# Kernel tuning notes

Measured on AMD Instinct MI355X. Metric: run time of the kernel, lower is better.

## Reference

```python
import jax, jax.numpy as jnp
import numpy as np

D = 256          # embedding_dim
N_SUPPORT = 320  # n_way * n_shot = 20 * 16
N_QUERY = 2048
N_WAY = 20


def setup_inputs() -> dict:
    key = jax.random.key(0)
    ks = jax.random.split(key, 6)
    scale = 1.0 / np.sqrt(2 * D)
    return {
        "support_embeddings": jax.random.normal(ks[0], (N_SUPPORT, D), dtype=jnp.float32),
        "query_embeddings": jax.random.normal(ks[1], (N_QUERY, D), dtype=jnp.float32),
        "support_labels": jax.random.randint(ks[2], (N_SUPPORT,), 0, N_WAY, dtype=jnp.int64)
            if jax.config.jax_enable_x64 else jax.random.randint(ks[2], (N_SUPPORT,), 0, N_WAY, dtype=jnp.int32),
        "W1": jax.random.normal(ks[3], (2 * D, D), dtype=jnp.float32) * scale,
        "b1": jax.random.normal(ks[4], (D,), dtype=jnp.float32) * scale,
        "W2": jax.random.normal(ks[5], (D,), dtype=jnp.float32) * (1.0 / np.sqrt(D)),
        "b2": jnp.zeros((1,), dtype=jnp.float32),
        "n_way": N_WAY,
        "n_shot": 16,
    }


def reference(support_embeddings, query_embeddings, support_labels, W1, b1, W2, b2, n_way, n_shot):
    d = support_embeddings.shape[-1]
    # Linear1 over concat([query, support]) == query @ W1[:d] + support @ W1[d:]
    q_proj = query_embeddings @ W1[:d]          # [Q, D]
    s_proj = support_embeddings @ W1[d:]        # [S, D]
    hidden = jax.nn.relu(q_proj[:, None, :] + s_proj[None, :, :] + b1)  # [Q, S, D]
    scores = jnp.einsum("qsd,d->qs", hidden, W2) + b2[0]                # [Q, S]
    weights = jax.nn.softmax(scores, axis=1)                            # softmax over support set
    onehot = jax.nn.one_hot(support_labels, n_way, dtype=weights.dtype) # [S, n_way]
    logits = weights @ onehot                                           # [Q, n_way]
    return logits
```

## Files before the change

### kernel.cpp

```cpp
#include <hip/hip_runtime.h>
#include <cstdint>

#define DD   256
#define NS   320
#define NQ   2048
#define NWAY 20
#define QT   4
#define SBLK 4
#define NQB  (NQ / QT)
#define NSB  (NS / SBLK)
#define MT   640

__global__ __launch_bounds__(256) void proj_kernel(
    const float* __restrict__ sup, const float* __restrict__ qe,
    const float* __restrict__ W1, const float* __restrict__ b1,
    float* __restrict__ qp, float* __restrict__ spbT) {
  const int d = threadIdx.x;
  const int b = blockIdx.x;
  if (b < NQB) {
    const int q0 = b * QT;
    float acc[QT] = {0.f, 0.f, 0.f, 0.f};
    const float* w = W1 + d;
#pragma unroll 8
    for (int k = 0; k < DD; ++k) {
      const float wv = w[(size_t)k * DD];
#pragma unroll
      for (int i = 0; i < QT; ++i)
        acc[i] += qe[(q0 + i) * DD + k] * wv;
    }
#pragma unroll
    for (int i = 0; i < QT; ++i)
      qp[(size_t)(q0 + i) * DD + d] = acc[i];
  } else {
    const int s0 = (b - NQB) * SBLK;
    float acc[SBLK] = {0.f, 0.f, 0.f, 0.f};
    const float* w = W1 + (size_t)DD * DD + d;
#pragma unroll 8
    for (int k = 0; k < DD; ++k) {
      const float wv = w[(size_t)k * DD];
#pragma unroll
      for (int i = 0; i < SBLK; ++i)
        acc[i] += sup[(s0 + i) * DD + k] * wv;
    }
    const float bb = b1[d];
#pragma unroll
    for (int i = 0; i < SBLK; ++i)
      spbT[d * NS + s0 + i] = acc[i] + bb;
  }
}

__global__ __launch_bounds__(MT) void matchnet_kernel(
    const float* __restrict__ qp, const float* __restrict__ spbT,
    const float* __restrict__ W2, const int* __restrict__ labels,
    float* __restrict__ out) {
  __shared__ float qlds[QT * DD];
  __shared__ float wlds[DD];
  __shared__ float part[QT][NS];
  __shared__ float lds_cs[QT * NWAY];
  __shared__ float lds_wm[5];
  const int t  = threadIdx.x;
  const int q0 = blockIdx.x * QT;

  if (t < QT * DD / 4) {
    ((float4*)qlds)[t] = ((const float4*)(qp + (size_t)q0 * DD))[t];
  } else if (t < QT * DD / 4 + DD / 4) {
    const int j = t - QT * DD / 4;
    ((float4*)wlds)[j] = ((const float4*)W2)[j];
  }
  if (t < QT * NWAY) lds_cs[t] = 0.f;
  __syncthreads();

  const int half = t / NS;
  const int s    = t - half * NS;
  const int d0   = half * (DD / 2);
  const int lab  = labels[s];

  float acc[QT] = {0.f, 0.f, 0.f, 0.f};
  const float* pS = spbT + d0 * NS + s;
#pragma unroll 2
  for (int dd = 0; dd < DD / 2; dd += 4) {
    const int d = d0 + dd;
    const float sv0 = pS[(dd + 0) * NS];
    const float sv1 = pS[(dd + 1) * NS];
    const float sv2 = pS[(dd + 2) * NS];
    const float sv3 = pS[(dd + 3) * NS];
    const float4 wv = *(const float4*)(wlds + d);
#pragma unroll
    for (int i = 0; i < QT; ++i) {
      const float4 qv = *(const float4*)(qlds + i * DD + d);
      acc[i] += fmaxf(qv.x + sv0, 0.f) * wv.x
              + fmaxf(qv.y + sv1, 0.f) * wv.y
              + fmaxf(qv.z + sv2, 0.f) * wv.z
              + fmaxf(qv.w + sv3, 0.f) * wv.w;
    }
  }

  if (half) {
#pragma unroll
    for (int i = 0; i < QT; ++i) part[i][s] = acc[i];
  }
  __syncthreads();
  if (!half) {
#pragma unroll
    for (int i = 0; i < QT; ++i) acc[i] += part[i][s];
    float m = acc[0];
#pragma unroll
    for (int i = 1; i < QT; ++i) m = fmaxf(m, acc[i]);
#pragma unroll
    for (int off = 32; off > 0; off >>= 1)
      m = fmaxf(m, __shfl_xor(m, off));
    if ((t & 63) == 0) lds_wm[t >> 6] = m;
  }
  __syncthreads();
  if (!half) {
    float M = lds_wm[0];
#pragma unroll
    for (int w = 1; w < 5; ++w) M = fmaxf(M, lds_wm[w]);
#pragma unroll
    for (int i = 0; i < QT; ++i) {
      const float w = __expf(acc[i] - M);
      atomicAdd(&lds_cs[i * NWAY + lab], w);
    }
  }
  __syncthreads();
  if (t < QT * NWAY) {
    const int i = t / NWAY, c = t - i * NWAY;
    float tot = 0.f;
#pragma unroll
    for (int j = 0; j < NWAY; ++j) tot += lds_cs[i * NWAY + j];
    out[(size_t)(q0 + i) * NWAY + c] = lds_cs[i * NWAY + c] / tot;
  }
}

extern "C" void kernel_launch(void* const* d_in, const int* in_sizes, int n_in,
                              void* d_out, int out_size, void* d_ws, size_t ws_size,
                              hipStream_t stream) {
  const float* sup = (const float*)d_in[0];
  const float* qe  = (const float*)d_in[1];
  const int*   lab = (const int*)d_in[2];
  const float* W1  = (const float*)d_in[3];
  const float* b1  = (const float*)d_in[4];
  const float* W2  = (const float*)d_in[5];
  float* out  = (float*)d_out;
  float* spbT = (float*)d_ws;
  float* qpr  = spbT + (size_t)DD * NS;

  proj_kernel<<<NQB + NSB, 256, 0, stream>>>(sup, qe, W1, b1, qpr, spbT);
  matchnet_kernel<<<NQ / QT, MT, 0, stream>>>(qpr, spbT, W2, lab, out);
}
```

Baseline: 103.2 us.

## Double query tile, split-K projection, scalar-load operands, bucket softmax by label

The query tile in both kernels grows from 4 to 8. That halves the number of matchnet blocks and doubles how often each support-projection load is reused. The projection kernel now splits the K dimension across two 256-thread halves and combines them through LDS. The matchnet kernel reads query and W2 values straight from global memory through wave-uniform (scalar) addresses instead of staging them in LDS. The per-class sum replaces the LDS atomic scatter with a label-bucket index list that is built once per block and then summed. The costs are more registers per thread, a hard CMAX=64 limit on support items per class, and a serial bucket-sum loop.

Result: no change. 101.7 us (-1.5%).

```diff
diff --git a/kernel.cpp b/kernel.cpp
--- a/kernel.cpp
+++ b/kernel.cpp
@@ -5,89 +5,91 @@
 #define NS   320
 #define NQ   2048
 #define NWAY 20
-#define QT   4
-#define SBLK 4
+#define QT   8
 #define NQB  (NQ / QT)
-#define NSB  (NS / SBLK)
-#define MT   640
+#define NSB  (NS / QT)
+#define CMAX 64
 
-__global__ __launch_bounds__(256) void proj_kernel(
+__global__ __launch_bounds__(512) void proj_kernel(
     const float* __restrict__ sup, const float* __restrict__ qe,
     const float* __restrict__ W1, const float* __restrict__ b1,
     float* __restrict__ qp, float* __restrict__ spbT) {
-  const int d = threadIdx.x;
-  const int b = blockIdx.x;
-  if (b < NQB) {
-    const int q0 = b * QT;
-    float acc[QT] = {0.f, 0.f, 0.f, 0.f};
-    const float* w = W1 + d;
+  __shared__ float pacc[QT][DD];
+  const int t  = threadIdx.x;
+  const int d  = t & 255;
+  const int kh = t >> 8;
+  const int b  = blockIdx.x;
+  const bool isQ = (b < NQB);
+  const int r0 = isQ ? b * QT : (b - NQB) * QT;
+  const float* src   = isQ ? qe : sup;
+  const float* wcol  = W1 + (isQ ? 0 : (size_t)DD * DD) + (size_t)(kh * 128) * DD + d;
+  const float* rbase = src + __builtin_amdgcn_readfirstlane(r0 * DD + kh * 128);
+
+  float acc[QT] = {0.f, 0.f, 0.f, 0.f, 0.f, 0.f, 0.f, 0.f};
 #pragma unroll 8
-    for (int k = 0; k < DD; ++k) {
-      const float wv = w[(size_t)k * DD];
+  for (int k = 0; k < 128; ++k) {
+    const float wv = wcol[(size_t)k * DD];
+#pragma unroll
+    for (int i = 0; i < QT; ++i)
+      acc[i] += rbase[i * DD + k] * wv;
+  }
+  if (kh) {
+#pragma unroll
+    for (int i = 0; i < QT; ++i) pacc[i][d] = acc[i];
+  }
+  __syncthreads();
+  if (!kh) {
+    if (isQ) {
 #pragma unroll
       for (int i = 0; i < QT; ++i)
-        acc[i] += qe[(q0 + i) * DD + k] * wv;
+        qp[(size_t)(r0 + i) * DD + d] = acc[i] + pacc[i][d];
+    } else {
+      const float bb = b1[d];
+#pragma unroll
+      for (int i = 0; i < QT; ++i)
+        spbT[d * NS + r0 + i] = acc[i] + pacc[i][d] + bb;
     }
-#pragma unroll
-    for (int i = 0; i < QT; ++i)
-      qp[(size_t)(q0 + i) * DD + d] = acc[i];
-  } else {
-    const int s0 = (b - NQB) * SBLK;
-    float acc[SBLK] = {0.f, 0.f, 0.f, 0.f};
-    const float* w = W1 + (size_t)DD * DD + d;
-#pragma unroll 8
-    for (int k = 0; k < DD; ++k) {
-      const float wv = w[(size_t)k * DD];
-#pragma unroll
-      for (int i = 0; i < SBLK; ++i)
-        acc[i] += sup[(s0 + i) * DD + k] * wv;
-    }
-    const float bb = b1[d];
-#pragma unroll
-    for (int i = 0; i < SBLK; ++i)
-      spbT[d * NS + s0 + i] = acc[i] + bb;
   }
 }
 
-__global__ __launch_bounds__(MT) void matchnet_kernel(
+__global__ __launch_bounds__(640) void matchnet_kernel(
     const float* __restrict__ qp, const float* __restrict__ spbT,
     const float* __restrict__ W2, const int* __restrict__ labels,
     float* __restrict__ out) {
-  __shared__ float qlds[QT * DD];
-  __shared__ float wlds[DD];
-  __shared__ float part[QT][NS];
-  __shared__ float lds_cs[QT * NWAY];
-  __shared__ float lds_wm[5];
-  const int t  = threadIdx.x;
-  const int q0 = blockIdx.x * QT;
-
-  if (t < QT * DD / 4) {
-    ((float4*)qlds)[t] = ((const float4*)(qp + (size_t)q0 * DD))[t];
-  } else if (t < QT * DD / 4 + DD / 4) {
-    const int j = t - QT * DD / 4;
-    ((float4*)wlds)[j] = ((const float4*)W2)[j];
-  }
-  if (t < QT * NWAY) lds_cs[t] = 0.f;
-  __syncthreads();
-
+  __shared__ float wexp[QT][NS];
+  __shared__ float wm[5];
+  __shared__ float csum[QT * NWAY];
+  __shared__ int   ccnt[NWAY];
+  __shared__ short cidx[NWAY * CMAX];
+  const int t    = threadIdx.x;
+  const int q0   = blockIdx.x * QT;
   const int half = t / NS;
   const int s    = t - half * NS;
-  const int d0   = half * (DD / 2);
-  const int lab  = labels[s];
 
-  float acc[QT] = {0.f, 0.f, 0.f, 0.f};
-  const float* pS = spbT + d0 * NS + s;
+  if (t < NWAY) ccnt[t] = 0;
+  __syncthreads();
+  if (!half) {
+    const int lab  = labels[s];
+    const int slot = atomicAdd(&ccnt[lab], 1);
+    cidx[lab * CMAX + slot] = (short)s;
+  }
+
+  const int d0 = half * (DD / 2);
+  const float* qb = qp + __builtin_amdgcn_readfirstlane(q0 * DD + d0);
+  const float* wb = W2 + d0;
+  const float* sb = spbT + (size_t)d0 * NS + s;
+
+  float acc[QT] = {0.f, 0.f, 0.f, 0.f, 0.f, 0.f, 0.f, 0.f};
 #pragma unroll 2
   for (int dd = 0; dd < DD / 2; dd += 4) {
-    const int d = d0 + dd;
-    const float sv0 = pS[(dd + 0) * NS];
-    const float sv1 = pS[(dd + 1) * NS];
-    const float sv2 = pS[(dd + 2) * NS];
-    const float sv3 = pS[(dd + 3) * NS];
-    const float4 wv = *(const float4*)(wlds + d);
+    const float sv0 = sb[(dd + 0) * NS];
+    const float sv1 = sb[(dd + 1) * NS];
+    const float sv2 = sb[(dd + 2) * NS];
+    const float sv3 = sb[(dd + 3) * NS];
+    const float4 wv = *(const float4*)(wb + dd);
 #pragma unroll
     for (int i = 0; i < QT; ++i) {
-      const float4 qv = *(const float4*)(qlds + i * DD + d);
+      const float4 qv = *(const float4*)(qb + i * DD + dd);
       acc[i] += fmaxf(qv.x + sv0, 0.f) * wv.x
               + fmaxf(qv.y + sv1, 0.f) * wv.y
               + fmaxf(qv.z + sv2, 0.f) * wv.z
@@ -97,38 +99,39 @@
 
   if (half) {
 #pragma unroll
-    for (int i = 0; i < QT; ++i) part[i][s] = acc[i];
+    for (int i = 0; i < QT; ++i) wexp[i][s] = acc[i];
+  }
+  __syncthreads();
+  float m = -1e30f;
+  if (!half) {
+#pragma unroll
+    for (int i = 0; i < QT; ++i) { acc[i] += wexp[i][s]; m = fmaxf(m, acc[i]); }
+#pragma unroll
+    for (int off = 32; off > 0; off >>= 1)
+      m = fmaxf(m, __shfl_xor(m, off));
+    if ((t & 63) == 0) wm[t >> 6] = m;
   }
   __syncthreads();
   if (!half) {
+    const float M = fmaxf(fmaxf(fmaxf(wm[0], wm[1]), fmaxf(wm[2], wm[3])), wm[4]);
 #pragma unroll
-    for (int i = 0; i < QT; ++i) acc[i] += part[i][s];
-    float m = acc[0];
-#pragma unroll
-    for (int i = 1; i < QT; ++i) m = fmaxf(m, acc[i]);
-#pragma unroll
-    for (int off = 32; off > 0; off >>= 1)
-      m = fmaxf(m, __shfl_xor(m, off));
-    if ((t & 63) == 0) lds_wm[t >> 6] = m;
+    for (int i = 0; i < QT; ++i) wexp[i][s] = __expf(acc[i] - M);
   }
   __syncthreads();
-  if (!half) {
-    float M = lds_wm[0];
-#pragma unroll
-    for (int w = 1; w < 5; ++w) M = fmaxf(M, lds_wm[w]);
-#pragma unroll
-    for (int i = 0; i < QT; ++i) {
-      const float w = __expf(acc[i] - M);
-      atomicAdd(&lds_cs[i * NWAY + lab], w);
-    }
+  if (t < QT * NWAY) {
+    const int i = t / NWAY, c = t - i * NWAY;
+    const int n = ccnt[c];
+    float sum = 0.f;
+    for (int j = 0; j < n; ++j) sum += wexp[i][cidx[c * CMAX + j]];
+    csum[t] = sum;
   }
   __syncthreads();
   if (t < QT * NWAY) {
     const int i = t / NWAY, c = t - i * NWAY;
     float tot = 0.f;
 #pragma unroll
-    for (int j = 0; j < NWAY; ++j) tot += lds_cs[i * NWAY + j];
-    out[(size_t)(q0 + i) * NWAY + c] = lds_cs[i * NWAY + c] / tot;
+    for (int j = 0; j < NWAY; ++j) tot += csum[i * NWAY + j];
+    out[(size_t)(q0 + i) * NWAY + c] = csum[t] / tot;
   }
 }
 
@@ -145,6 +148,6 @@
   float* spbT = (float*)d_ws;
   float* qpr  = spbT + (size_t)DD * NS;
 
-  proj_kernel<<<NQB + NSB, 256, 0, stream>>>(sup, qe, W1, b1, qpr, spbT);
-  matchnet_kernel<<<NQ / QT, MT, 0, stream>>>(qpr, spbT, W2, lab, out);
+  proj_kernel<<<NQB + NSB, 512, 0, stream>>>(sup, qe, W1, b1, qpr, spbT);
+  matchnet_kernel<<<NQ / QT, 640, 0, stream>>>(qpr, spbT, W2, lab, out);
 }
```
